# Optimization experiments

Measured on AMD Instinct MI355X. Metric: run time of the kernel, lower is better.

The kernel has to match this reference:

```python
import jax, jax.numpy as jnp
import numpy as np

DIM = 128
HEADS = 4
LOGIT_MAX = float(np.log(1.0 / 0.01))  # log(100)


def setup_inputs() -> dict:
    root = jax.random.key(0)
    ks = jax.random.split(root, 10)
    B, nH, nW, Lq, Lv, C = 16, 16, 16, 64, 64, DIM
    s = 0.02
    return {
        "query": jax.random.normal(ks[0], (B, nH, nW, Lq, C), jnp.float32),
        "key": jax.random.normal(ks[1], (B, nH, nW, Lv, C), jnp.float32),
        "value": jax.random.normal(ks[2], (B, nH, nW, Lv, C), jnp.float32),
        "position": jax.random.normal(ks[3], (B, HEADS, Lq, Lv), jnp.float32),
        # torch nn.Linear convention: weight [out_features, in_features]
        "Wq": jax.random.normal(ks[4], (C, C), jnp.float32) * s,
        "bq": jnp.zeros((C,), jnp.float32),
        "Wk": jax.random.normal(ks[5], (C, C), jnp.float32) * s,  # fc_key has no bias
        "Wv": jax.random.normal(ks[6], (C, C), jnp.float32) * s,
        "bv": jnp.zeros((C,), jnp.float32),
        "Wp": jax.random.normal(ks[7], (C, C), jnp.float32) * s,
        "bp": jnp.zeros((C,), jnp.float32),
        "logit_scale": jnp.log(10.0) * jnp.ones((HEADS, 1, 1), jnp.float32),
    }


def reference(query, key, value, position, Wq, bq, Wk, Wv, bv, Wp, bp, logit_scale):
    B, nH, nW, Lq, C = query.shape
    Lv = key.shape[3]
    H = logit_scale.shape[0]
    d = C // H
    # QKV projections, split heads: [B,nH,nW,H,L,d]
    q = (query @ Wq.T + bq).reshape(B, nH, nW, Lq, H, d).swapaxes(3, 4)
    k = (key @ Wk.T).reshape(B, nH, nW, Lv, H, d).swapaxes(3, 4)
    v = (value @ Wv.T + bv).reshape(B, nH, nW, Lv, H, d).swapaxes(3, 4)
    # clamped learned per-head logit scale
    scale = jnp.exp(jnp.minimum(logit_scale, LOGIT_MAX))  # [H,1,1]
    attn = jnp.einsum('bijhqd,bijhkd->bijhqk', q, k) * scale
    attn = attn + position[:, None, None]  # broadcast over window grid (nH,nW)
    attn = jax.nn.softmax(attn, axis=-1)
    x = jnp.einsum('bijhqk,bijhkd->bijhqd', attn, v)
    x = x.swapaxes(3, 4).reshape(B, nH, nW, Lq, C)
    x = x @ Wp.T + bp
    return (x, attn)
```

## Files before the change

kernel.cpp:

```cpp
#include <hip/hip_runtime.h>

using f16   = _Float16;
using f16x4 = __attribute__((ext_vector_type(4))) _Float16;
using f16x8 = __attribute__((ext_vector_type(8))) _Float16;
using f32x4 = __attribute__((ext_vector_type(4))) float;

#define DEVI __device__ __forceinline__

namespace {
constexpr int S_XQ  = 0;
constexpr int S_XK  = 16384;
constexpr int S_XV  = 32768;
constexpr int S_SCR = 49152;
constexpr float LOGIT_MAX_C = 4.6051701859880914f;
constexpr float L2E = 1.4426950408889634f;
}

DEVI int swzA(int row, int b) { return (row << 8) + (b ^ ((row & 7) << 4)); }
DEVI int swz64(int row, int b) { return (row << 6) + (b ^ (((row >> 1) & 3) << 4)); }

DEVI f16x8 ldA(const char* base, int row, int k0) {
  return *reinterpret_cast<const f16x8*>(base + swzA(row, k0 << 1));
}

DEVI void stage_in(const float* __restrict__ src, char* __restrict__ dst, int tid) {
#pragma unroll
  for (int i = 0; i < 8; ++i) {
    int f = tid + (i << 8);
    float4 v = reinterpret_cast<const float4*>(src)[f];
    f16x4 h;
    h[0] = (f16)v.x; h[1] = (f16)v.y; h[2] = (f16)v.z; h[3] = (f16)v.w;
    *reinterpret_cast<f16x4*>(dst + swzA(f >> 5, (f & 31) << 3)) = h;
  }
}

DEVI void proj_acc(const char* __restrict__ xb, const f16* __restrict__ Wm,
                   f32x4 (&acc)[4][2], int w, int lr, int lg) {
#pragma unroll
  for (int mt = 0; mt < 4; ++mt)
#pragma unroll
    for (int n = 0; n < 2; ++n)
      acc[mt][n] = f32x4{0.f, 0.f, 0.f, 0.f};
#pragma unroll
  for (int kt = 0; kt < 4; ++kt) {
    f16x8 b0 = *reinterpret_cast<const f16x8*>(Wm + (w * 32 + lr) * 128 + kt * 32 + lg * 8);
    f16x8 b1 = *reinterpret_cast<const f16x8*>(Wm + (w * 32 + 16 + lr) * 128 + kt * 32 + lg * 8);
#pragma unroll
    for (int mt = 0; mt < 4; ++mt) {
      f16x8 a = ldA(xb, mt * 16 + lr, kt * 32 + lg * 8);
      acc[mt][0] = __builtin_amdgcn_mfma_f32_16x16x32_f16(a, b0, acc[mt][0], 0, 0, 0);
      acc[mt][1] = __builtin_amdgcn_mfma_f32_16x16x32_f16(a, b1, acc[mt][1], 0, 0, 0);
    }
  }
}

DEVI void epi_scr64(const f32x4 (&acc)[4][2], char* __restrict__ scr,
                    const float* __restrict__ bias, int lr, int lg) {
  float b0 = bias ? bias[lr] : 0.f;
  float b1 = bias ? bias[16 + lr] : 0.f;
#pragma unroll
  for (int mt = 0; mt < 4; ++mt)
#pragma unroll
    for (int n = 0; n < 2; ++n)
#pragma unroll
      for (int r = 0; r < 4; ++r) {
        int row = mt * 16 + lg * 4 + r;
        *reinterpret_cast<f16*>(scr + swz64(row, (n * 16 + lr) << 1)) =
            (f16)(acc[mt][n][r] + (n ? b1 : b0));
      }
}
DEVI f16x8 ldS64(const char* __restrict__ scr, int row, int lg) {
  return *reinterpret_cast<const f16x8*>(scr + swz64(row, lg << 4));
}

DEVI void epi_rowmajor(const f32x4 (&acc)[4][2], char* __restrict__ dst,
                       int w, int lr, int lg) {
#pragma unroll
  for (int mt = 0; mt < 4; ++mt)
#pragma unroll
    for (int n = 0; n < 2; ++n)
#pragma unroll
      for (int r = 0; r < 4; ++r) {
        int row = mt * 16 + lg * 4 + r;
        int col = w * 32 + n * 16 + lr;
        *reinterpret_cast<f16*>(dst + swzA(row, col << 1)) = (f16)acc[mt][n][r];
      }
}

__global__ void wcvt_kernel(const float* __restrict__ Wq, const float* __restrict__ Wk,
                            const float* __restrict__ Wv, const float* __restrict__ Wp,
                            f16* __restrict__ W16) {
  int idx = blockIdx.x * 256 + threadIdx.x;
  int m = idx >> 12;
  int off = (idx & 4095) << 2;
  const float* src = m == 0 ? Wq : m == 1 ? Wk : m == 2 ? Wv : Wp;
  float4 v = *reinterpret_cast<const float4*>(src + off);
  f16x4 h;
  h[0] = (f16)v.x; h[1] = (f16)v.y; h[2] = (f16)v.z; h[3] = (f16)v.w;
  *reinterpret_cast<f16x4*>(W16 + (m << 14) + off) = h;
}

__global__ __launch_bounds__(256, 2)
void fpca_kernel(const float* __restrict__ q_in, const float* __restrict__ k_in,
                 const float* __restrict__ v_in, const float* __restrict__ pos_in,
                 const f16* __restrict__ W16,
                 const float* __restrict__ bq, const float* __restrict__ bv,
                 const float* __restrict__ bp, const float* __restrict__ lsc,
                 float* __restrict__ d_x, float* __restrict__ d_attn) {
  __shared__ char smem[81920];
  const int tid = threadIdx.x;
  const int w = tid >> 6;
  const int lane = tid & 63;
  const int lr = lane & 15;
  const int lg = lane >> 4;
  const int win = blockIdx.x;
  const int b = win >> 8;
  const size_t winOff = (size_t)win << 13;
  const f16* Wq16 = W16;
  const f16* Wk16 = W16 + 16384;
  const f16* Wv16 = W16 + 32768;
  const f16* Wp16 = W16 + 49152;
  char* scr = smem + S_SCR + (w << 13);

  stage_in(q_in + winOff, smem + S_XQ, tid);
  stage_in(k_in + winOff, smem + S_XK, tid);
  stage_in(v_in + winOff, smem + S_XV, tid);
  __syncthreads();

  f32x4 acc[4][2];
  proj_acc(smem + S_XQ, Wq16, acc, w, lr, lg);
  epi_scr64(acc, scr, bq + w * 32, lr, lg);
  f16x8 bQ[4];
#pragma unroll
  for (int nt = 0; nt < 4; ++nt) bQ[nt] = ldS64(scr, nt * 16 + lr, lg);

  proj_acc(smem + S_XK, Wk16, acc, w, lr, lg);
  epi_scr64(acc, scr + 4096, nullptr, lr, lg);
  f16x8 aK[4];
#pragma unroll
  for (int mt = 0; mt < 4; ++mt) aK[mt] = ldS64(scr + 4096, mt * 16 + lr, lg);

  const float scale = exp2f(fminf(lsc[w], LOGIT_MAX_C) * L2E);
  const float* pos = pos_in + (((size_t)b * 4 + w) << 12);
  float* attn_out = d_attn + (((size_t)win * 4 + w) << 12);
  f16x4 P16[4][4];
#pragma unroll
  for (int nt = 0; nt < 4; ++nt) {
    f32x4 s[4];
#pragma unroll
    for (int mt = 0; mt < 4; ++mt) s[mt] = f32x4{0.f, 0.f, 0.f, 0.f};
#pragma unroll
    for (int mt = 0; mt < 4; ++mt)
      s[mt] = __builtin_amdgcn_mfma_f32_16x16x32_f16(aK[mt], bQ[nt], s[mt], 0, 0, 0);
    const int q = nt * 16 + lr;
#pragma unroll
    for (int mt = 0; mt < 4; ++mt) {
      float4 pv = *reinterpret_cast<const float4*>(pos + (q << 6) + mt * 16 + lg * 4);
      s[mt][0] = s[mt][0] * scale + pv.x;
      s[mt][1] = s[mt][1] * scale + pv.y;
      s[mt][2] = s[mt][2] * scale + pv.z;
      s[mt][3] = s[mt][3] * scale + pv.w;
    }
    float m = s[0][0];
#pragma unroll
    for (int mt = 0; mt < 4; ++mt)
#pragma unroll
      for (int r = 0; r < 4; ++r) m = fmaxf(m, s[mt][r]);
    m = fmaxf(m, __shfl_xor(m, 16));
    m = fmaxf(m, __shfl_xor(m, 32));
    float sum = 0.f;
#pragma unroll
    for (int mt = 0; mt < 4; ++mt)
#pragma unroll
      for (int r = 0; r < 4; ++r) {
        float e = exp2f((s[mt][r] - m) * L2E);
        s[mt][r] = e;
        sum += e;
      }
    sum += __shfl_xor(sum, 16);
    sum += __shfl_xor(sum, 32);
    float rinv = __builtin_amdgcn_rcpf(sum);
#pragma unroll
    for (int mt = 0; mt < 4; ++mt) {
      float4 o;
      o.x = (s[mt][0] *= rinv);
      o.y = (s[mt][1] *= rinv);
      o.z = (s[mt][2] *= rinv);
      o.w = (s[mt][3] *= rinv);
      *reinterpret_cast<float4*>(attn_out + (q << 6) + mt * 16 + lg * 4) = o;
      P16[mt][nt][0] = (f16)s[mt][0];
      P16[mt][nt][1] = (f16)s[mt][1];
      P16[mt][nt][2] = (f16)s[mt][2];
      P16[mt][nt][3] = (f16)s[mt][3];
    }
  }

#pragma unroll
  for (int mt = 0; mt < 4; ++mt)
#pragma unroll
    for (int nt = 0; nt < 4; ++nt) {
      const int q = nt * 16 + lr;
      *reinterpret_cast<f16x4*>(scr + (q << 7) +
          ((mt * 32 + lg * 8) ^ ((lr & 7) << 4))) = P16[mt][nt];
    }
  f16x8 aP[4][2];
#pragma unroll
  for (int mt = 0; mt < 4; ++mt)
#pragma unroll
    for (int kt = 0; kt < 2; ++kt) {
      const int q = mt * 16 + lr;
      aP[mt][kt] = *reinterpret_cast<const f16x8*>(scr + (q << 7) +
          ((kt * 64 + lg * 16) ^ ((lr & 7) << 4)));
    }

  proj_acc(smem + S_XV, Wv16, acc, w, lr, lg);
  {
    float c0 = bv[w * 32 + lr], c1 = bv[w * 32 + 16 + lr];
#pragma unroll
    for (int mt = 0; mt < 4; ++mt)
#pragma unroll
      for (int n = 0; n < 2; ++n) {
        int co = n * 16 + lr;
        f16x4 h;
        h[0] = (f16)(acc[mt][n][0] + (n ? c1 : c0));
        h[1] = (f16)(acc[mt][n][1] + (n ? c1 : c0));
        h[2] = (f16)(acc[mt][n][2] + (n ? c1 : c0));
        h[3] = (f16)(acc[mt][n][3] + (n ? c1 : c0));
        *reinterpret_cast<f16x4*>(scr + (co << 7) +
            ((mt * 32 + lg * 8) ^ ((lr & 7) << 4))) = h;
      }
  }
  f16x8 bV[2][2];
#pragma unroll
  for (int n = 0; n < 2; ++n)
#pragma unroll
    for (int kt = 0; kt < 2; ++kt) {
      int d = n * 16 + lr;
      bV[n][kt] = *reinterpret_cast<const f16x8*>(scr + (d << 7) +
          ((kt * 64 + lg * 16) ^ ((lr & 7) << 4)));
    }

  f32x4 oacc[4][2];
#pragma unroll
  for (int mt = 0; mt < 4; ++mt)
#pragma unroll
    for (int n = 0; n < 2; ++n)
      oacc[mt][n] = f32x4{0.f, 0.f, 0.f, 0.f};
#pragma unroll
  for (int mt = 0; mt < 4; ++mt)
#pragma unroll
    for (int kt = 0; kt < 2; ++kt) {
      oacc[mt][0] = __builtin_amdgcn_mfma_f32_16x16x32_f16(aP[mt][kt], bV[0][kt], oacc[mt][0], 0, 0, 0);
      oacc[mt][1] = __builtin_amdgcn_mfma_f32_16x16x32_f16(aP[mt][kt], bV[1][kt], oacc[mt][1], 0, 0, 0);
    }

  __syncthreads();
  epi_rowmajor(oacc, smem + S_XQ, w, lr, lg);
  __syncthreads();

  f32x4 xacc[4][2];
  proj_acc(smem + S_XQ, Wp16, xacc, w, lr, lg);
  const float b0 = bp[w * 32 + lr];
  const float b1 = bp[w * 32 + 16 + lr];
  float* xo = d_x + winOff;
#pragma unroll
  for (int mt = 0; mt < 4; ++mt)
#pragma unroll
    for (int n = 0; n < 2; ++n)
#pragma unroll
      for (int r = 0; r < 4; ++r) {
        int row = mt * 16 + lg * 4 + r;
        int col = w * 32 + n * 16 + lr;
        xo[(row << 7) + col] = xacc[mt][n][r] + (n ? b1 : b0);
      }
}

extern "C" void kernel_launch(void* const* d_in, const int* in_sizes, int n_in,
                              void* d_out, int out_size, void* d_ws, size_t ws_size,
                              hipStream_t stream) {
  const float* q   = (const float*)d_in[0];
  const float* k   = (const float*)d_in[1];
  const float* v   = (const float*)d_in[2];
  const float* pos = (const float*)d_in[3];
  const float* Wq  = (const float*)d_in[4];
  const float* bq  = (const float*)d_in[5];
  const float* Wk  = (const float*)d_in[6];
  const float* Wv  = (const float*)d_in[7];
  const float* bv  = (const float*)d_in[8];
  const float* Wp  = (const float*)d_in[9];
  const float* bp  = (const float*)d_in[10];
  const float* ls  = (const float*)d_in[11];
  f16* W16 = (f16*)d_ws;
  float* d_x    = (float*)d_out;
  float* d_attn = d_x + (size_t)16 * 16 * 16 * 64 * 128;
  wcvt_kernel<<<64, 256, 0, stream>>>(Wq, Wk, Wv, Wp, W16);
  fpca_kernel<<<4096, 256, 0, stream>>>(q, k, v, pos, W16, bq, bv, bp, ls,
                                        d_x, d_attn);
}
```

Before: 212.5 us.

## Shrink LDS footprint to fit three workgroups per CU

Cuts shared memory from 80KB to 48KB. The value tile is now prefetched into registers as f16 and written into the key buffer once K is consumed, and the per-wave scratch is halved by writing the P matrix in two halves. Launch bounds move to 3 blocks per CU so more windows are resident at once to hide memory latency. The cost is more register pressure from the prefetch buffer, a possible spill under the tighter register budget, and an extra barrier.

```diff
diff --git a/kernel.cpp b/kernel.cpp
--- a/kernel.cpp
+++ b/kernel.cpp
@@ -10,8 +10,7 @@
 namespace {
 constexpr int S_XQ  = 0;
 constexpr int S_XK  = 16384;
-constexpr int S_XV  = 32768;
-constexpr int S_SCR = 49152;
+constexpr int S_SCR = 32768;
 constexpr float LOGIT_MAX_C = 4.6051701859880914f;
 constexpr float L2E = 1.4426950408889634f;
 }
@@ -100,14 +99,14 @@
   *reinterpret_cast<f16x4*>(W16 + (m << 14) + off) = h;
 }
 
-__global__ __launch_bounds__(256, 2)
+__global__ __launch_bounds__(256, 3)
 void fpca_kernel(const float* __restrict__ q_in, const float* __restrict__ k_in,
                  const float* __restrict__ v_in, const float* __restrict__ pos_in,
                  const f16* __restrict__ W16,
                  const float* __restrict__ bq, const float* __restrict__ bv,
                  const float* __restrict__ bp, const float* __restrict__ lsc,
                  float* __restrict__ d_x, float* __restrict__ d_attn) {
-  __shared__ char smem[81920];
+  __shared__ char smem[49152];
   const int tid = threadIdx.x;
   const int w = tid >> 6;
   const int lane = tid & 63;
@@ -120,11 +119,18 @@
   const f16* Wk16 = W16 + 16384;
   const f16* Wv16 = W16 + 32768;
   const f16* Wp16 = W16 + 49152;
-  char* scr = smem + S_SCR + (w << 13);
+  char* scr = smem + S_SCR + (w << 12);
 
   stage_in(q_in + winOff, smem + S_XQ, tid);
   stage_in(k_in + winOff, smem + S_XK, tid);
-  stage_in(v_in + winOff, smem + S_XV, tid);
+  const float4* vsrc = reinterpret_cast<const float4*>(v_in + winOff);
+  f16x4 pfh[8];
+#pragma unroll
+  for (int i = 0; i < 8; ++i) {
+    float4 v = vsrc[tid + (i << 8)];
+    pfh[i][0] = (f16)v.x; pfh[i][1] = (f16)v.y;
+    pfh[i][2] = (f16)v.z; pfh[i][3] = (f16)v.w;
+  }
   __syncthreads();
 
   f32x4 acc[4][2];
@@ -135,10 +141,17 @@
   for (int nt = 0; nt < 4; ++nt) bQ[nt] = ldS64(scr, nt * 16 + lr, lg);
 
   proj_acc(smem + S_XK, Wk16, acc, w, lr, lg);
-  epi_scr64(acc, scr + 4096, nullptr, lr, lg);
+  epi_scr64(acc, scr, nullptr, lr, lg);
   f16x8 aK[4];
 #pragma unroll
-  for (int mt = 0; mt < 4; ++mt) aK[mt] = ldS64(scr + 4096, mt * 16 + lr, lg);
+  for (int mt = 0; mt < 4; ++mt) aK[mt] = ldS64(scr, mt * 16 + lr, lg);
+  __syncthreads();
+
+#pragma unroll
+  for (int i = 0; i < 8; ++i) {
+    int f = tid + (i << 8);
+    *reinterpret_cast<f16x4*>(smem + S_XK + swzA(f >> 5, (f & 31) << 3)) = pfh[i];
+  }
 
   const float scale = exp2f(fminf(lsc[w], LOGIT_MAX_C) * L2E);
   const float* pos = pos_in + (((size_t)b * 4 + w) << 12);
@@ -195,39 +208,44 @@
     }
   }
 
-#pragma unroll
-  for (int mt = 0; mt < 4; ++mt)
-#pragma unroll
-    for (int nt = 0; nt < 4; ++nt) {
-      const int q = nt * 16 + lr;
-      *reinterpret_cast<f16x4*>(scr + (q << 7) +
-          ((mt * 32 + lg * 8) ^ ((lr & 7) << 4))) = P16[mt][nt];
-    }
+#define WR_P(MT)                                                                   \
+  {                                                                                \
+    _Pragma("unroll") for (int nt = 0; nt < 4; ++nt) {                             \
+      const int q = nt * 16 + lr;                                                  \
+      *reinterpret_cast<f16x4*>(scr + (q << 6) +                                   \
+          (((((MT) & 1) << 5) + (lg << 3)) ^ (((q >> 1) & 3) << 4))) =             \
+          P16[MT][nt];                                                             \
+    }                                                                              \
+  }
   f16x8 aP[4][2];
 #pragma unroll
-  for (int mt = 0; mt < 4; ++mt)
-#pragma unroll
-    for (int kt = 0; kt < 2; ++kt) {
+  for (int h = 0; h < 2; ++h) {
+    WR_P(2 * h)
+    WR_P(2 * h + 1)
+#pragma unroll
+    for (int mt = 0; mt < 4; ++mt) {
       const int q = mt * 16 + lr;
-      aP[mt][kt] = *reinterpret_cast<const f16x8*>(scr + (q << 7) +
-          ((kt * 64 + lg * 16) ^ ((lr & 7) << 4)));
-    }
-
-  proj_acc(smem + S_XV, Wv16, acc, w, lr, lg);
+      aP[mt][h] = *reinterpret_cast<const f16x8*>(scr + (q << 6) +
+          ((lg << 4) ^ (((q >> 1) & 3) << 4)));
+    }
+  }
+  __syncthreads();
+
+  proj_acc(smem + S_XK, Wv16, acc, w, lr, lg);
   {
     float c0 = bv[w * 32 + lr], c1 = bv[w * 32 + 16 + lr];
 #pragma unroll
     for (int mt = 0; mt < 4; ++mt)
 #pragma unroll
       for (int n = 0; n < 2; ++n) {
-        int co = n * 16 + lr;
+        int d = n * 16 + lr;
         f16x4 h;
         h[0] = (f16)(acc[mt][n][0] + (n ? c1 : c0));
         h[1] = (f16)(acc[mt][n][1] + (n ? c1 : c0));
         h[2] = (f16)(acc[mt][n][2] + (n ? c1 : c0));
         h[3] = (f16)(acc[mt][n][3] + (n ? c1 : c0));
-        *reinterpret_cast<f16x4*>(scr + (co << 7) +
-            ((mt * 32 + lg * 8) ^ ((lr & 7) << 4))) = h;
+        *reinterpret_cast<f16x4*>(scr + (d << 7) +
+            ((mt * 32 + lg * 8) ^ ((d & 7) << 4))) = h;
       }
   }
   f16x8 bV[2][2];
@@ -237,7 +255,7 @@
     for (int kt = 0; kt < 2; ++kt) {
       int d = n * 16 + lr;
       bV[n][kt] = *reinterpret_cast<const f16x8*>(scr + (d << 7) +
-          ((kt * 64 + lg * 16) ^ ((lr & 7) << 4)));
+          ((kt * 64 + lg * 16) ^ ((d & 7) << 4)));
     }
 
   f32x4 oacc[4][2];
@@ -254,7 +272,6 @@
       oacc[mt][1] = __builtin_amdgcn_mfma_f32_16x16x32_f16(aP[mt][kt], bV[1][kt], oacc[mt][1], 0, 0, 0);
     }
 
-  __syncthreads();
   epi_rowmajor(oacc, smem + S_XQ, w, lr, lg);
   __syncthreads();
 
```

Measured after the change: 205.6 us. -3.3%, faster.
